# Performance work log

Measured on AMD Instinct MI355X. Metric: run time of the kernel, lower is better.

Reference implementation:

```python
import jax, jax.numpy as jnp
import numpy as np

N_NODES = 65536
N_EDGES = 524288
N_GRAPHS = 512
G_NODES = 10000
NUM_DISEASES = 2000
IN_DIM = 128
HID = 256  # 2 * IN_DIM (z_emb concat feat)
D_FEAT = 512
C_FEAT = 512
MAX_Z = 4000


def setup_inputs() -> dict:
    key = jax.random.key(0)
    ks = jax.random.split(key, 20)
    rn = lambda k, shape: jax.random.normal(k, shape, dtype=jnp.float32) * 0.05
    return {
        "z": jax.random.randint(ks[0], (N_NODES,), 0, MAX_Z),
        "node_id": jnp.sort(jax.random.randint(ks[1], (N_NODES,), 0, G_NODES)),
        "src": jax.random.randint(ks[2], (N_EDGES,), 0, N_NODES),
        "dst": jax.random.randint(ks[3], (N_EDGES,), 0, N_NODES),
        "graph_ids": jnp.sort(jax.random.randint(ks[4], (N_NODES,), 0, N_GRAPHS)),
        "z_table": rn(ks[5], (MAX_Z, IN_DIM)),
        "d_feat_tab": rn(ks[6], (G_NODES, D_FEAT)),
        "c_feat_tab": rn(ks[7], (G_NODES, C_FEAT)),
        "Wd": rn(ks[8], (D_FEAT, IN_DIM)),
        "Wc": rn(ks[9], (C_FEAT, IN_DIM)),
        "gin_W1": rn(ks[10], (HID, HID)), "gin_b1": jnp.zeros((HID,), jnp.float32),
        "gin_W2": rn(ks[11], (HID, HID)), "gin_b2": jnp.zeros((HID,), jnp.float32),
        "sage_Wself": rn(ks[12], (HID, HID)),
        "sage_Wneigh": rn(ks[13], (HID, HID)),
        "sage_b": jnp.zeros((HID,), jnp.float32),
        "lin1_W": rn(ks[14], (HID, HID)), "lin1_b": jnp.zeros((HID,), jnp.float32),
        "lin2_W": rn(ks[15], (HID, 1)), "lin2_b": jnp.zeros((1,), jnp.float32),
    }


def reference(z, node_id, src, dst, graph_ids, z_table, d_feat_tab, c_feat_tab,
              Wd, Wc, gin_W1, gin_b1, gin_W2, gin_b2,
              sage_Wself, sage_Wneigh, sage_b, lin1_W, lin1_b, lin2_W, lin2_b):
    # --- input feature construction (Model.forward) ---
    z_emb = z_table[z]                               # [N, IN_DIM]
    d_proj = d_feat_tab[node_id] @ Wd                # d_fc (bias=False)
    c_proj = c_feat_tab[node_id] @ Wc                # c_fc (bias=False)
    disease = (node_id <= NUM_DISEASES)[:, None]
    # node_id is sorted -> masked concat order == node order
    feat = jnp.where(disease, d_proj, c_proj)        # [N, IN_DIM]
    x = jnp.concatenate([z_emb, feat], axis=1)       # [N, HID]
    # --- GINConv: sum aggregation, eps=0, mlp = Lin->ReLU->Lin ---
    agg = jax.ops.segment_sum(x[src], dst, num_segments=N_NODES)
    h = x + agg
    h = jax.nn.relu(h @ gin_W1 + gin_b1) @ gin_W2 + gin_b2
    # --- SAGEConv('mean'): fc_self(h) + fc_neigh(mean_neighbors) + bias ---
    deg = jax.ops.segment_sum(jnp.ones((N_EDGES,), h.dtype), dst, num_segments=N_NODES)
    mean_n = jax.ops.segment_sum(h[src], dst, num_segments=N_NODES) / jnp.maximum(deg, 1.0)[:, None]
    h = h @ sage_Wself + mean_n @ sage_Wneigh + sage_b
    # --- per-graph max pooling readout ---
    g = jax.ops.segment_max(h, graph_ids, num_segments=N_GRAPHS, indices_are_sorted=True)
    g = jnp.where(jnp.isfinite(g), g, 0.0)           # guard empty graphs
    # --- head: Linear -> ReLU -> (dropout p=0, eval) -> Linear ---
    h = jax.nn.relu(g @ lin1_W + lin1_b)
    return h @ lin2_W + lin2_b                       # [N_GRAPHS, 1]
```

## Files before the change

kernel.cpp:

```cpp
#include <hip/hip_runtime.h>
#include <hip/hip_bf16.h>

#define N_NODES     65536
#define N_EDGES     524288
#define N_GRAPHS    512
#define G_NODES_N   10000
#define NUM_DIS     2000
#define IN_DIM      128
#define HID         256
#define D_FEAT      512
#define MAX_Z       4000

typedef _Float16 half8 __attribute__((ext_vector_type(8)));
typedef float    f32x4 __attribute__((ext_vector_type(4)));

typedef __attribute__((address_space(1))) const void as1_void;
typedef __attribute__((address_space(3))) void       as3_void;

__global__ __launch_bounds__(256) void prep_kernel(
    const float* __restrict__ Ws, const float* __restrict__ Wn,
    const float* __restrict__ Wd, const float* __restrict__ Wc,
    const float* __restrict__ W1, const float* __restrict__ W2,
    const float* __restrict__ z_table,
    const int* __restrict__ z, const int* __restrict__ node_id,
    _Float16* __restrict__ WsT, _Float16* __restrict__ WnT,
    _Float16* __restrict__ WdT, _Float16* __restrict__ WcT,
    _Float16* __restrict__ W12P, _Float16* __restrict__ zt16,
    int2* __restrict__ zn2, int* __restrict__ cnt, int* __restrict__ flags)
{
    const int b = blockIdx.x;
    const int tid = threadIdx.x;
    if (b < 64) {
        __shared__ float tile[64][65];
        const float* W; _Float16* T; int K, N, k0, n0;
        if (b < 32) {
            const int mat = b >> 4, t = b & 15;
            K = HID; N = HID; k0 = (t >> 2) * 64; n0 = (t & 3) * 64;
            W = (mat == 0) ? Ws : Wn;
            T = (mat == 0) ? WsT : WnT;
        } else {
            const int bb = b - 32;
            const int mat = bb >> 4, t = bb & 15;
            K = D_FEAT; N = IN_DIM; k0 = (t >> 1) * 64; n0 = (t & 1) * 64;
            W = (mat == 0) ? Wd : Wc;
            T = (mat == 0) ? WdT : WcT;
        }
        const int tx = tid & 63, ty = tid >> 6;
        #pragma unroll
        for (int r = 0; r < 64; r += 4)
            tile[r + ty][tx] = W[(size_t)(k0 + r + ty) * N + n0 + tx];
        __syncthreads();
        #pragma unroll
        for (int c = 0; c < 64; c += 4)
            T[(size_t)(n0 + c + ty) * K + k0 + tx] = (_Float16)tile[tx][c + ty];
    } else if (b < 576) {
        const int bb = b - 64;
        const int mat = bb >> 8;
        const int k = bb & 255;
        const int n = tid;
        const float* W = mat ? W2 : W1;
        const float v = W[(size_t)k * HID + n];
        const size_t idx = (size_t)(mat * 8 + (k >> 5)) * 8192
                         + (size_t)((((k >> 3) & 3) * 256 + n) * 8 + (k & 7));
        W12P[idx] = (_Float16)v;
    } else if (b < 826) {
        const size_t base = ((size_t)(b - 576) * 256 + tid) * 8;
        const float4 f0 = *(const float4*)(z_table + base);
        const float4 f1 = *(const float4*)(z_table + base + 4);
        half8 h;
        h[0]=(_Float16)f0.x; h[1]=(_Float16)f0.y; h[2]=(_Float16)f0.z; h[3]=(_Float16)f0.w;
        h[4]=(_Float16)f1.x; h[5]=(_Float16)f1.y; h[6]=(_Float16)f1.z; h[7]=(_Float16)f1.w;
        *(half8*)(zt16 + base) = h;
    } else if (b < 890) {
        const int base = (b - 826) * 1024 + tid * 4;
        *(int4*)(cnt + base) = make_int4(0, 0, 0, 0);
        if (b == 826 && tid < 128) flags[tid] = 0;
    } else {
        const int i = (b - 890) * 256 + tid;
        zn2[i] = make_int2(z[i] << 8, node_id[i] << 8);
    }
}

__global__ __launch_bounds__(256) void proj_hist_kernel(
    const float* __restrict__ dtab, const float* __restrict__ ctab,
    const _Float16* __restrict__ WdT, const _Float16* __restrict__ WcT,
    _Float16* __restrict__ proj,
    const int* __restrict__ dst, int* __restrict__ cnt)
{
    const int blk = blockIdx.x;
    if (blk >= 79) {
        const int e = (blk - 79) * 256 + threadIdx.x;
        if (e < N_EDGES) atomicAdd(&cnt[dst[e]], 1);
        return;
    }
    __shared__ _Float16 Alds[128 * 40];
    __shared__ _Float16 Blds[128 * 40];
    const float* tab; const _Float16* WT; int base, M, bm;
    if (blk < 16) { tab = dtab; WT = WdT; base = 0;           M = NUM_DIS + 1;             bm = blk * 128; }
    else          { tab = ctab; WT = WcT; base = NUM_DIS + 1; M = G_NODES_N - NUM_DIS - 1; bm = (blk - 16) * 128; }
    const int tid  = threadIdx.x;
    const int wave = tid >> 6, lane = tid & 63;
    const int q    = lane >> 4, l16 = lane & 15;
    const int mbase = (wave & 1) * 64, nbase = (wave >> 1) * 64;
    const int r = tid >> 1, s = tid & 1;

    f32x4 acc[4][4] = {};

    for (int kc = 0; kc < 16; ++kc) {
        const int k0 = kc * 32;
        const int arow = min(bm + r, M - 1);
        const float* gA = tab + (size_t)(base + arow) * D_FEAT + k0 + s * 16;
        const _Float16* gB = WT + (size_t)r * D_FEAT + k0 + s * 16;
        const float4 f0 = ((const float4*)gA)[0];
        const float4 f1 = ((const float4*)gA)[1];
        const float4 f2 = ((const float4*)gA)[2];
        const float4 f3 = ((const float4*)gA)[3];
        const half8 hb0 = *(const half8*)gB;
        const half8 hb1 = *(const half8*)(gB + 8);
        half8 h0, h1;
        h0[0]=(_Float16)f0.x; h0[1]=(_Float16)f0.y; h0[2]=(_Float16)f0.z; h0[3]=(_Float16)f0.w;
        h0[4]=(_Float16)f1.x; h0[5]=(_Float16)f1.y; h0[6]=(_Float16)f1.z; h0[7]=(_Float16)f1.w;
        h1[0]=(_Float16)f2.x; h1[1]=(_Float16)f2.y; h1[2]=(_Float16)f2.z; h1[3]=(_Float16)f2.w;
        h1[4]=(_Float16)f3.x; h1[5]=(_Float16)f3.y; h1[6]=(_Float16)f3.z; h1[7]=(_Float16)f3.w;
        __syncthreads();
        *(half8*)&Alds[r * 40 + s * 16]     = h0;
        *(half8*)&Alds[r * 40 + s * 16 + 8] = h1;
        *(half8*)&Blds[r * 40 + s * 16]     = hb0;
        *(half8*)&Blds[r * 40 + s * 16 + 8] = hb1;
        __syncthreads();
        half8 a[4], b[4];
        #pragma unroll
        for (int i = 0; i < 4; ++i)
            a[i] = *(const half8*)&Alds[(mbase + i * 16 + l16) * 40 + q * 8];
        #pragma unroll
        for (int j = 0; j < 4; ++j)
            b[j] = *(const half8*)&Blds[(nbase + j * 16 + l16) * 40 + q * 8];
        #pragma unroll
        for (int i = 0; i < 4; ++i)
            #pragma unroll
            for (int j = 0; j < 4; ++j)
                acc[i][j] = __builtin_amdgcn_mfma_f32_16x16x32_f16(a[i], b[j], acc[i][j], 0, 0, 0);
    }

    #pragma unroll
    for (int j = 0; j < 4; ++j) {
        const int colg = nbase + j * 16 + l16;
        #pragma unroll
        for (int i = 0; i < 4; ++i) {
            #pragma unroll
            for (int rr = 0; rr < 4; ++rr) {
                const int row = bm + mbase + i * 16 + q * 4 + rr;
                if (row < M)
                    proj[(size_t)(base + row) * IN_DIM + colg] = (_Float16)acc[i][j][rr];
            }
        }
    }
}

__global__ __launch_bounds__(256) void scan_fused_kernel(
    const int* __restrict__ cnt, int* __restrict__ row_ptr,
    int* __restrict__ fill, int* __restrict__ flags,
    const int2* __restrict__ zn2, int2* __restrict__ pzn,
    int2* __restrict__ prbe, int* __restrict__ pnode,
    int* __restrict__ bhist)
{
    __shared__ int a[256], b[256];
    __shared__ int sums[64];
    __shared__ int segbase;
    __shared__ int hist[64];
    __shared__ int pos[64];
    const int t = threadIdx.x;
    const int blk = blockIdx.x;
    const int base = blk * 1024 + t * 4;
    const int4 c = *(const int4*)(cnt + base);
    const int s = c.x + c.y + c.z + c.w;
    a[t] = s;
    if (t < 64) hist[t] = 0;
    __syncthreads();
    int* in = a; int* out = b;
    for (int off = 1; off < 256; off <<= 1) {
        out[t] = in[t] + ((t >= off) ? in[t - off] : 0);
        __syncthreads();
        int* tmp = in; in = out; out = tmp;
    }
    if (t == 0) {
        atomicExch(&flags[64 + blk], in[255]);
        __threadfence();
        atomicAdd(&flags[0], 1);
        while (atomicAdd(&flags[0], 0) < 64) {}
    }
    __syncthreads();
    if (t < 64) sums[t] = atomicAdd(&flags[64 + t], 0);
    __syncthreads();
    if (t == 0) {
        int pfx = 0;
        for (int i = 0; i < blk; ++i) pfx += sums[i];
        segbase = pfx;
        if (blk == 63) {
            int tot = pfx;
            for (int i = blk; i < 64; ++i) tot += sums[i];
            row_ptr[N_NODES] = tot;
        }
    }
    __syncthreads();
    const int run = in[t] - s + segbase;
    int4 r;
    r.x = run; r.y = run + c.x; r.z = r.y + c.y; r.w = r.z + c.z;
    *(int4*)(row_ptr + base) = r;
    *(int4*)(fill + base) = r;

    const int bk0 = min(c.x, 63), bk1 = min(c.y, 63);
    const int bk2 = min(c.z, 63), bk3 = min(c.w, 63);
    atomicAdd(&hist[bk0], 1); atomicAdd(&hist[bk1], 1);
    atomicAdd(&hist[bk2], 1); atomicAdd(&hist[bk3], 1);
    __syncthreads();
    if (t < 64) bhist[blk * 64 + t] = hist[t];
    __threadfence();
    if (t == 0) {
        atomicAdd(&flags[1], 1);
        while (atomicAdd(&flags[1], 0) < 64) {}
    }
    __syncthreads();
    if (t < 64) {
        int pre = 0, tot = 0;
        for (int i = 0; i < 64; ++i) {
            const int v = atomicAdd(&bhist[i * 64 + t], 0);
            if (i < blk) pre += v;
            tot += v;
        }
        hist[t] = tot;
        pos[t] = pre;
    }
    __syncthreads();
    if (t == 0) {
        int run2 = 0;
        for (int i = 0; i < 64; ++i) { const int tt = hist[i]; hist[i] = run2; run2 += tt; }
    }
    __syncthreads();
    if (t < 64) pos[t] = hist[t] + pos[t];
    __syncthreads();
    const int begs[4] = { r.x, r.y, r.z, r.w };
    const int ends[4] = { r.y, r.z, r.w, r.w + c.w };
    const int bks[4]  = { bk0, bk1, bk2, bk3 };
    #pragma unroll
    for (int k = 0; k < 4; ++k) {
        const int p = atomicAdd(&pos[bks[k]], 1);
        pzn[p]   = zn2[base + k];
        prbe[p]  = make_int2(begs[k], ends[k]);
        pnode[p] = base + k;
    }
}

__global__ __launch_bounds__(256) void scatter_kernel(
    const int* __restrict__ src, const int* __restrict__ dst,
    const int2* __restrict__ zn2,
    int* __restrict__ fill, int* __restrict__ col, int2* __restrict__ colzn)
{
    const int e = blockIdx.x * 256 + threadIdx.x;
    if (e < N_EDGES) {
        const int s = src[e];
        const int pos = atomicAdd(&fill[dst[e]], 1);
        col[pos] = s;
        colzn[pos] = zn2[s];
    }
}

__global__ __launch_bounds__(256) void gin_fused_kernel(
    const int2* __restrict__ prbe, const int2* __restrict__ colzn,
    const int2* __restrict__ pzn, const int* __restrict__ pnode,
    const _Float16* __restrict__ zt16, const _Float16* __restrict__ proj,
    const _Float16* __restrict__ W12P,
    const float* __restrict__ b1, const float* __restrict__ b2,
    _Float16* __restrict__ H)
{
    __shared__ _Float16 Apanel[64 * 264];
    __shared__ _Float16 Blds[8192];
    __shared__ int prows[64];

    const int bm   = blockIdx.x * 64;
    const int tid  = threadIdx.x;
    const int wave = tid >> 6, lane = tid & 63;
    const int q    = lane >> 4, l16 = lane & 15;
    const int nbase = wave * 64;
    const int sb   = wave * 256 + lane;

    if (tid < 64) prows[tid] = pnode[bm + tid];

    #pragma unroll
    for (int tt = 0; tt < 4; ++tt) {
        const int seg = (wave * 4 + tt) * 64 + lane;
        __builtin_amdgcn_global_load_lds((as1_void*)(W12P + seg * 8),
            (as3_void*)&Blds[(wave * 4 + tt) * 64 * 8], 16, 0, 0);
    }

    {
        const int p = tid & 7;
        const char* ztb = (const char*)zt16 + p * 32;
        const char* prb = (const char*)proj + p * 32;
        #pragma unroll 1
        for (int pass = 0; pass < 2; ++pass) {
            const int r  = (tid >> 3) + (pass << 5);
            const int gr = bm + r;
            const int2 be = prbe[gr];
            const int beg = be.x, end = be.y;
            float za[16], pa[16];
            {
                const int2 zn = pzn[gr];
                const half8* zp = (const half8*)(ztb + zn.x);
                const half8* pp = (const half8*)(prb + zn.y);
                const half8 z0 = zp[0], z1 = zp[1], p0 = pp[0], p1 = pp[1];
                #pragma unroll
                for (int i = 0; i < 8; ++i) {
                    za[i] = (float)z0[i]; za[8 + i] = (float)z1[i];
                    pa[i] = (float)p0[i]; pa[8 + i] = (float)p1[i];
                }
            }
            int e = beg;
            int2 iA, iB, iC, iD;
            if (e + 4 <= end) {
                iA = colzn[e]; iB = colzn[e + 1]; iC = colzn[e + 2]; iD = colzn[e + 3];
            }
            for (; e + 4 <= end; e += 4) {
                const half8* zpA = (const half8*)(ztb + iA.x);
                const half8* ppA = (const half8*)(prb + iA.y);
                const half8* zpB = (const half8*)(ztb + iB.x);
                const half8* ppB = (const half8*)(prb + iB.y);
                const half8* zpC = (const half8*)(ztb + iC.x);
                const half8* ppC = (const half8*)(prb + iC.y);
                const half8* zpD = (const half8*)(ztb + iD.x);
                const half8* ppD = (const half8*)(prb + iD.y);
                const half8 zA0 = zpA[0], zA1 = zpA[1], pA0 = ppA[0], pA1 = ppA[1];
                const half8 zB0 = zpB[0], zB1 = zpB[1], pB0 = ppB[0], pB1 = ppB[1];
                const half8 zC0 = zpC[0], zC1 = zpC[1], pC0 = ppC[0], pC1 = ppC[1];
                const half8 zD0 = zpD[0], zD1 = zpD[1], pD0 = ppD[0], pD1 = ppD[1];
                if (e + 8 <= end) {
                    iA = colzn[e + 4]; iB = colzn[e + 5];
                    iC = colzn[e + 6]; iD = colzn[e + 7];
                }
                #pragma unroll
                for (int i = 0; i < 8; ++i) {
                    za[i]     += ((float)zA0[i] + (float)zB0[i]) + ((float)zC0[i] + (float)zD0[i]);
                    za[8 + i] += ((float)zA1[i] + (float)zB1[i]) + ((float)zC1[i] + (float)zD1[i]);
                    pa[i]     += ((float)pA0[i] + (float)pB0[i]) + ((float)pC0[i] + (float)pD0[i]);
                    pa[8 + i] += ((float)pA1[i] + (float)pB1[i]) + ((float)pC1[i] + (float)pD1[i]);
                }
            }
            for (; e + 2 <= end; e += 2) {
                const int2 jA = colzn[e];
                const int2 jB = colzn[e + 1];
                const half8* zpA = (const half8*)(ztb + jA.x);
                const half8* ppA = (const half8*)(prb + jA.y);
                const half8* zpB = (const half8*)(ztb + jB.x);
                const half8* ppB = (const half8*)(prb + jB.y);
                const half8 zA0 = zpA[0], zA1 = zpA[1], pA0 = ppA[0], pA1 = ppA[1];
                const half8 zB0 = zpB[0], zB1 = zpB[1], pB0 = ppB[0], pB1 = ppB[1];
                #pragma unroll
                for (int i = 0; i < 8; ++i) {
                    za[i]     += (float)zA0[i] + (float)zB0[i];
                    za[8 + i] += (float)zA1[i] + (float)zB1[i];
                    pa[i]     += (float)pA0[i] + (float)pB0[i];
                    pa[8 + i] += (float)pA1[i] + (float)pB1[i];
                }
            }
            if (e < end) {
                const int2 jA = colzn[e];
                const half8* zp = (const half8*)(ztb + jA.x);
                const half8* pp = (const half8*)(prb + jA.y);
                const half8 z0 = zp[0], z1 = zp[1], p0 = pp[0], p1 = pp[1];
                #pragma unroll
                for (int i = 0; i < 8; ++i) {
                    za[i] += (float)z0[i]; za[8 + i] += (float)z1[i];
                    pa[i] += (float)p0[i]; pa[8 + i] += (float)p1[i];
                }
            }
            half8 oz0, oz1, op0, op1;
            #pragma unroll
            for (int i = 0; i < 8; ++i) {
                oz0[i] = (_Float16)za[i];     oz1[i] = (_Float16)za[8 + i];
                op0[i] = (_Float16)pa[i];     op1[i] = (_Float16)pa[8 + i];
            }
            *(half8*)&Apanel[r * 264 + p * 16]           = oz0;
            *(half8*)&Apanel[r * 264 + p * 16 + 8]       = oz1;
            *(half8*)&Apanel[r * 264 + 128 + p * 16]     = op0;
            *(half8*)&Apanel[r * 264 + 128 + p * 16 + 8] = op1;
        }
    }
    __syncthreads();

    half8 pf0, pf1, pf2, pf3;
    auto pfetch = [&](int c) {
        const _Float16* s = W12P + (size_t)c * 8192 + (size_t)sb * 8;
        pf0 = *(const half8*)(s);
        pf1 = *(const half8*)(s + 512);
        pf2 = *(const half8*)(s + 1024);
        pf3 = *(const half8*)(s + 1536);
    };
    pfetch(1);

    f32x4 acc[4][4] = {};
    for (int c = 0; c < 16; ++c) {
        const int kl = (c & 7) * 32;
        half8 a[4], b[4];
        #pragma unroll
        for (int i = 0; i < 4; ++i)
            a[i] = *(const half8*)&Apanel[(i * 16 + l16) * 264 + kl + q * 8];
        #pragma unroll
        for (int j = 0; j < 4; ++j)
            b[j] = *(const half8*)&Blds[(q * 256 + nbase + j * 16 + l16) * 8];
        #pragma unroll
        for (int i = 0; i < 4; ++i)
            #pragma unroll
            for (int j = 0; j < 4; ++j)
                acc[i][j] = __builtin_amdgcn_mfma_f32_16x16x32_f16(a[i], b[j], acc[i][j], 0, 0, 0);
        if (c == 15) break;
        __syncthreads();
        *(half8*)&Blds[sb * 8]         = pf0;
        *(half8*)&Blds[(sb + 64) * 8]  = pf1;
        *(half8*)&Blds[(sb + 128) * 8] = pf2;
        *(half8*)&Blds[(sb + 192) * 8] = pf3;
        if (c == 7) {
            #pragma unroll
            for (int j = 0; j < 4; ++j) {
                const int colg = nbase + j * 16 + l16;
                const float bv = b1[colg];
                #pragma unroll
                for (int i = 0; i < 4; ++i)
                    #pragma unroll
                    for (int rr = 0; rr < 4; ++rr) {
                        const float v = fmaxf(acc[i][j][rr] + bv, 0.0f);
                        Apanel[(i * 16 + q * 4 + rr) * 264 + colg] = (_Float16)v;
                        acc[i][j][rr] = 0.0f;
                    }
            }
        }
        if (c < 14) pfetch(c + 2);
        __syncthreads();
    }

    #pragma unroll
    for (int j = 0; j < 4; ++j) {
        const int colg = nbase + j * 16 + l16;
        const float bv = b2[colg];
        #pragma unroll
        for (int i = 0; i < 4; ++i)
            #pragma unroll
            for (int rr = 0; rr < 4; ++rr) {
                const int rowl = i * 16 + q * 4 + rr;
                H[(size_t)prows[rowl] * HID + colg] = (_Float16)(acc[i][j][rr] + bv);
            }
    }
}

__global__ __launch_bounds__(256) void csr_agg_kernel(
    const int2* __restrict__ prbe, const int* __restrict__ pnode,
    const int* __restrict__ col,
    const _Float16* __restrict__ F, _Float16* __restrict__ OUT)
{
    const int t = blockIdx.x * 256 + threadIdx.x;
    const int i = t >> 5;
    const int q = t & 31;
    const int2 be = prbe[i];
    const int beg = be.x, end = be.y;
    float acc[8] = {0.f,0.f,0.f,0.f,0.f,0.f,0.f,0.f};
    int e = beg;
    for (; e + 8 <= end; e += 8) {
        const int s0 = col[e],     s1 = col[e + 1];
        const int s2 = col[e + 2], s3 = col[e + 3];
        const int s4 = col[e + 4], s5 = col[e + 5];
        const int s6 = col[e + 6], s7 = col[e + 7];
        const half8 v0 = *(const half8*)(F + (size_t)s0 * HID + q * 8);
        const half8 v1 = *(const half8*)(F + (size_t)s1 * HID + q * 8);
        const half8 v2 = *(const half8*)(F + (size_t)s2 * HID + q * 8);
        const half8 v3 = *(const half8*)(F + (size_t)s3 * HID + q * 8);
        const half8 v4 = *(const half8*)(F + (size_t)s4 * HID + q * 8);
        const half8 v5 = *(const half8*)(F + (size_t)s5 * HID + q * 8);
        const half8 v6 = *(const half8*)(F + (size_t)s6 * HID + q * 8);
        const half8 v7 = *(const half8*)(F + (size_t)s7 * HID + q * 8);
        #pragma unroll
        for (int k = 0; k < 8; ++k)
            acc[k] += (((float)v0[k] + (float)v1[k]) + ((float)v2[k] + (float)v3[k]))
                    + (((float)v4[k] + (float)v5[k]) + ((float)v6[k] + (float)v7[k]));
    }
    for (; e + 4 <= end; e += 4) {
        const int s0 = col[e],     s1 = col[e + 1];
        const int s2 = col[e + 2], s3 = col[e + 3];
        const half8 v0 = *(const half8*)(F + (size_t)s0 * HID + q * 8);
        const half8 v1 = *(const half8*)(F + (size_t)s1 * HID + q * 8);
        const half8 v2 = *(const half8*)(F + (size_t)s2 * HID + q * 8);
        const half8 v3 = *(const half8*)(F + (size_t)s3 * HID + q * 8);
        #pragma unroll
        for (int k = 0; k < 8; ++k)
            acc[k] += ((float)v0[k] + (float)v1[k]) + ((float)v2[k] + (float)v3[k]);
    }
    for (; e < end; ++e) {
        const half8 v0 = *(const half8*)(F + (size_t)col[e] * HID + q * 8);
        #pragma unroll
        for (int k = 0; k < 8; ++k) acc[k] += (float)v0[k];
    }
    const float rs = 1.0f / fmaxf((float)(end - beg), 1.0f);
    half8 o;
    #pragma unroll
    for (int k = 0; k < 8; ++k) o[k] = (_Float16)(acc[k] * rs);
    const int d = pnode[i];
    *(half8*)(OUT + (size_t)d * HID + q * 8) = o;
}

__global__ __launch_bounds__(256) void mfma_gemm_kernel(
    const _Float16* __restrict__ A1, const _Float16* __restrict__ A2,
    const _Float16* __restrict__ B1T, const _Float16* __restrict__ B2T,
    const float* __restrict__ bias, _Float16* __restrict__ Ch)
{
    __shared__ _Float16 Alds[128 * 32];
    __shared__ _Float16 Blds[128 * 32];
    const int bm   = blockIdx.x * 128;
    const int bn   = blockIdx.y * 128;
    const int tid  = threadIdx.x;
    const int wave = tid >> 6, lane = tid & 63;
    const int q    = lane >> 4, l16 = lane & 15;
    const int mbase = (wave & 1) * 64, nbase = (wave >> 1) * 64;

    const int i0 = wave * 128 + lane;
    const int i1 = i0 + 64;
    const int r0 = i0 >> 2, s0 = i0 & 3;
    const int r1 = i1 >> 2, s1 = i1 & 3;

    half8 pa0, pa1, pb0, pb1;
    auto pfetch = [&](int kc) {
        const int k0 = (kc & 7) * 32;
        const _Float16* Ab = (kc < 8) ? A1 : A2;
        const _Float16* Bb = (kc < 8) ? B1T : B2T;
        pa0 = *(const half8*)(Ab + (size_t)(bm + r0) * HID + k0 + s0 * 8);
        pa1 = *(const half8*)(Ab + (size_t)(bm + r1) * HID + k0 + s1 * 8);
        pb0 = *(const half8*)(Bb + (size_t)(bn + r0) * HID + k0 + s0 * 8);
        pb1 = *(const half8*)(Bb + (size_t)(bn + r1) * HID + k0 + s1 * 8);
    };
    pfetch(0);

    f32x4 acc[4][4] = {};

    for (int kc = 0; kc < 16; ++kc) {
        __syncthreads();
        *(half8*)&Alds[i0 * 8] = pa0;
        *(half8*)&Alds[i1 * 8] = pa1;
        *(half8*)&Blds[i0 * 8] = pb0;
        *(half8*)&Blds[i1 * 8] = pb1;
        if (kc < 15) pfetch(kc + 1);
        __syncthreads();
        half8 a[4], b[4];
        #pragma unroll
        for (int i = 0; i < 4; ++i)
            a[i] = *(const half8*)&Alds[(mbase + i * 16 + l16) * 32 + q * 8];
        #pragma unroll
        for (int j = 0; j < 4; ++j)
            b[j] = *(const half8*)&Blds[(nbase + j * 16 + l16) * 32 + q * 8];
        #pragma unroll
        for (int i = 0; i < 4; ++i)
            #pragma unroll
            for (int j = 0; j < 4; ++j)
                acc[i][j] = __builtin_amdgcn_mfma_f32_16x16x32_f16(a[i], b[j], acc[i][j], 0, 0, 0);
    }

    #pragma unroll
    for (int j = 0; j < 4; ++j) {
        const int colg = bn + nbase + j * 16 + l16;
        const float bv = bias[colg];
        #pragma unroll
        for (int i = 0; i < 4; ++i) {
            #pragma unroll
            for (int rr = 0; rr < 4; ++rr) {
                const int rowg = bm + mbase + i * 16 + q * 4 + rr;
                Ch[(size_t)rowg * HID + colg] = (_Float16)(acc[i][j][rr] + bv);
            }
        }
    }
}

__global__ __launch_bounds__(256) void pool_head_kernel(
    const _Float16* __restrict__ H2, const int* __restrict__ gid,
    const float* __restrict__ W1, const float* __restrict__ b1,
    const float* __restrict__ W2, const float* __restrict__ b2,
    float* __restrict__ out)
{
    const int g = blockIdx.x;
    const int tid = threadIdx.x;
    int lo = 0, hi = N_NODES;
    while (lo < hi) { const int mid = (lo + hi) >> 1; if (gid[mid] < g) lo = mid + 1; else hi = mid; }
    const int start = lo;
    hi = N_NODES;
    while (lo < hi) { const int mid = (lo + hi) >> 1; if (gid[mid] < g + 1) lo = mid + 1; else hi = mid; }
    const int end = lo;

    const int rowofs = tid >> 5;
    const int q = tid & 31;
    float m8[8];
    #pragma unroll
    for (int k = 0; k < 8; ++k) m8[k] = -INFINITY;
    for (int i = start + rowofs; i < end; i += 8) {
        const half8 v = *(const half8*)(H2 + (size_t)i * HID + q * 8);
        #pragma unroll
        for (int k = 0; k < 8; ++k) m8[k] = fmaxf(m8[k], (float)v[k]);
    }
    __shared__ float part[8][256];
    #pragma unroll
    for (int k = 0; k < 8; ++k) part[rowofs][q * 8 + k] = m8[k];
    __syncthreads();
    __shared__ float row[HID];
    __shared__ float red[HID];
    const int j = tid;
    float m = part[0][j];
    #pragma unroll
    for (int r = 1; r < 8; ++r) m = fmaxf(m, part[r][j]);
    row[j] = (m == -INFINITY) ? 0.0f : m;
    __syncthreads();
    float acc = b1[j];
    #pragma unroll 8
    for (int k = 0; k < HID; ++k)
        acc = fmaf(row[k], W1[k * HID + j], acc);
    acc = fmaxf(acc, 0.f);
    red[j] = acc * W2[j];
    __syncthreads();
    for (int s = 128; s > 0; s >>= 1) {
        if (j < s) red[j] += red[j + s];
        __syncthreads();
    }
    if (j == 0) out[g] = red[0] + b2[0];
}

extern "C" void kernel_launch(void* const* d_in, const int* in_sizes, int n_in,
                              void* d_out, int out_size, void* d_ws, size_t ws_size,
                              hipStream_t stream)
{
    const int*   z         = (const int*)d_in[0];
    const int*   node_id   = (const int*)d_in[1];
    const int*   src       = (const int*)d_in[2];
    const int*   dst       = (const int*)d_in[3];
    const int*   graph_ids = (const int*)d_in[4];
    const float* z_table   = (const float*)d_in[5];
    const float* d_feat    = (const float*)d_in[6];
    const float* c_feat    = (const float*)d_in[7];
    const float* Wd        = (const float*)d_in[8];
    const float* Wc        = (const float*)d_in[9];
    const float* gin_W1    = (const float*)d_in[10];
    const float* gin_b1    = (const float*)d_in[11];
    const float* gin_W2    = (const float*)d_in[12];
    const float* gin_b2    = (const float*)d_in[13];
    const float* sage_Wself  = (const float*)d_in[14];
    const float* sage_Wneigh = (const float*)d_in[15];
    const float* sage_b    = (const float*)d_in[16];
    const float* lin1_W    = (const float*)d_in[17];
    const float* lin1_b    = (const float*)d_in[18];
    const float* lin2_W    = (const float*)d_in[19];
    const float* lin2_b    = (const float*)d_in[20];
    float* out = (float*)d_out;

    const size_t NH = (size_t)N_NODES * HID;
    char* wsb = (char*)d_ws;
    _Float16* Hh   = (_Float16*)wsb;                     wsb += NH * 2;
    _Float16* AGGh = (_Float16*)wsb;                     wsb += NH * 2;
    _Float16* H2h  = (_Float16*)wsb;                     wsb += NH * 2;
    _Float16* projh= (_Float16*)wsb;                     wsb += (size_t)G_NODES_N * IN_DIM * 2;
    _Float16* W12P = (_Float16*)wsb;                     wsb += 16 * 8192 * 2;
    _Float16* WsT  = (_Float16*)wsb;                     wsb += HID * HID * 2;
    _Float16* WnT  = (_Float16*)wsb;                     wsb += HID * HID * 2;
    _Float16* WdT  = (_Float16*)wsb;                     wsb += D_FEAT * IN_DIM * 2;
    _Float16* WcT  = (_Float16*)wsb;                     wsb += D_FEAT * IN_DIM * 2;
    _Float16* zt16 = (_Float16*)wsb;                     wsb += (size_t)MAX_Z * IN_DIM * 2;
    int2* zn2      = (int2*)wsb;                         wsb += (size_t)N_NODES * 8;
    int2* colzn    = (int2*)wsb;                         wsb += (size_t)(N_EDGES + 8) * 8;
    int2* pzn      = (int2*)wsb;                         wsb += (size_t)N_NODES * 8;
    int2* prbe     = (int2*)wsb;                         wsb += (size_t)N_NODES * 8;
    int* pnode     = (int*)wsb;                          wsb += (size_t)N_NODES * 4;
    int* bhist     = (int*)wsb;                          wsb += 64 * 64 * 4;
    int* row_ptr   = (int*)wsb;                          wsb += (N_NODES + 4) * 4;
    int* cnt       = (int*)wsb;                          wsb += N_NODES * 4;
    int* fill      = (int*)wsb;                          wsb += N_NODES * 4;
    int* col       = (int*)wsb;                          wsb += N_EDGES * 4;
    int* flags     = (int*)wsb;                          wsb += 128 * 4;

    prep_kernel<<<1146, 256, 0, stream>>>(
        sage_Wself, sage_Wneigh, Wd, Wc, gin_W1, gin_W2, z_table, z, node_id,
        WsT, WnT, WdT, WcT, W12P, zt16, zn2, cnt, flags);

    proj_hist_kernel<<<79 + N_EDGES / 256, 256, 0, stream>>>(
        d_feat, c_feat, WdT, WcT, projh, dst, cnt);

    scan_fused_kernel<<<64, 256, 0, stream>>>(
        cnt, row_ptr, fill, flags, zn2, pzn, prbe, pnode, bhist);
    scatter_kernel<<<N_EDGES / 256, 256, 0, stream>>>(src, dst, zn2, fill, col, colzn);

    gin_fused_kernel<<<N_NODES / 64, 256, 0, stream>>>(
        prbe, colzn, pzn, pnode, zt16, projh, W12P, gin_b1, gin_b2, Hh);

    csr_agg_kernel<<<(N_NODES * 32) / 256, 256, 0, stream>>>(
        prbe, pnode, col, Hh, AGGh);

    dim3 ggrid(N_NODES / 128, HID / 128);
    mfma_gemm_kernel<<<ggrid, 256, 0, stream>>>(Hh, AGGh, WsT, WnT, sage_b, H2h);

    pool_head_kernel<<<N_GRAPHS, 256, 0, stream>>>(
        H2h, graph_ids, lin1_W, lin1_b, lin2_W, lin2_b, out);
}
```

Baseline: 348.6 us.

## Split GIN gather out of fused MLP kernel into separate gather pass

Moves the neighbor-sum aggregation of the GIN layer out of the fused gather+MLP kernel into a dedicated gather kernel that uses 16 lanes per node, with z-embedding and projection halves handled by different lanes. The aggregated fp16 rows are written to a new workspace buffer and then loaded into LDS by the MLP kernel. The aim is more parallelism and better latency hiding for the irregular gathers, which previously ran with only 8 threads per row inside the LDS-heavy MLP kernel. The cost is an extra global round trip of a 65536x256 fp16 buffer and one more kernel launch.

```diff
diff --git a/kernel.cpp b/kernel.cpp
--- a/kernel.cpp
+++ b/kernel.cpp
@@ -265,10 +265,68 @@
     }
 }
 
-__global__ __launch_bounds__(256) void gin_fused_kernel(
-    const int2* __restrict__ prbe, const int2* __restrict__ colzn,
-    const int2* __restrict__ pzn, const int* __restrict__ pnode,
+__global__ __launch_bounds__(256, 6) void gather_kernel(
+    const int2* __restrict__ prbe, const int2* __restrict__ pzn,
+    const int2* __restrict__ colzn,
     const _Float16* __restrict__ zt16, const _Float16* __restrict__ proj,
+    _Float16* __restrict__ AGG)
+{
+    const int i = blockIdx.x * 16 + (threadIdx.x >> 4);
+    const int l = threadIdx.x & 15;
+    const bool isz = (l < 8);
+    const char* tab = isz ? (const char*)zt16 : (const char*)proj;
+    const int loff = (l & 7) * 32;
+    const int2 be = prbe[i];
+    const int2 zn = pzn[i];
+    float acc[16];
+    {
+        const half8* sp = (const half8*)(tab + (isz ? zn.x : zn.y) + loff);
+        const half8 v0 = sp[0], v1 = sp[1];
+        #pragma unroll
+        for (int k = 0; k < 8; ++k) { acc[k] = (float)v0[k]; acc[8 + k] = (float)v1[k]; }
+    }
+    int e = be.x;
+    const int end = be.y;
+    int2 iA, iB, iC, iD;
+    if (e + 4 <= end) {
+        iA = colzn[e]; iB = colzn[e + 1]; iC = colzn[e + 2]; iD = colzn[e + 3];
+    }
+    for (; e + 4 <= end; e += 4) {
+        const half8* sA = (const half8*)(tab + (isz ? iA.x : iA.y) + loff);
+        const half8* sB = (const half8*)(tab + (isz ? iB.x : iB.y) + loff);
+        const half8* sC = (const half8*)(tab + (isz ? iC.x : iC.y) + loff);
+        const half8* sD = (const half8*)(tab + (isz ? iD.x : iD.y) + loff);
+        const half8 a0 = sA[0], a1 = sA[1];
+        const half8 b0 = sB[0], b1 = sB[1];
+        const half8 c0 = sC[0], c1 = sC[1];
+        const half8 d0 = sD[0], d1 = sD[1];
+        if (e + 8 <= end) {
+            iA = colzn[e + 4]; iB = colzn[e + 5];
+            iC = colzn[e + 6]; iD = colzn[e + 7];
+        }
+        #pragma unroll
+        for (int k = 0; k < 8; ++k) {
+            acc[k]     += ((float)a0[k] + (float)b0[k]) + ((float)c0[k] + (float)d0[k]);
+            acc[8 + k] += ((float)a1[k] + (float)b1[k]) + ((float)c1[k] + (float)d1[k]);
+        }
+    }
+    for (; e < end; ++e) {
+        const int2 j = colzn[e];
+        const half8* s = (const half8*)(tab + (isz ? j.x : j.y) + loff);
+        const half8 v0 = s[0], v1 = s[1];
+        #pragma unroll
+        for (int k = 0; k < 8; ++k) { acc[k] += (float)v0[k]; acc[8 + k] += (float)v1[k]; }
+    }
+    half8 o0, o1;
+    #pragma unroll
+    for (int k = 0; k < 8; ++k) { o0[k] = (_Float16)acc[k]; o1[k] = (_Float16)acc[8 + k]; }
+    _Float16* dst = AGG + (size_t)i * 256 + l * 16;
+    *(half8*)dst = o0;
+    *(half8*)(dst + 8) = o1;
+}
+
+__global__ __launch_bounds__(256) void gin_mlp_kernel(
+    const _Float16* __restrict__ AGG, const int* __restrict__ pnode,
     const _Float16* __restrict__ W12P,
     const float* __restrict__ b1, const float* __restrict__ b2,
     _Float16* __restrict__ H)
@@ -294,96 +352,14 @@
     }
 
     {
-        const int p = tid & 7;
-        const char* ztb = (const char*)zt16 + p * 32;
-        const char* prb = (const char*)proj + p * 32;
-        #pragma unroll 1
-        for (int pass = 0; pass < 2; ++pass) {
-            const int r  = (tid >> 3) + (pass << 5);
-            const int gr = bm + r;
-            const int2 be = prbe[gr];
-            const int beg = be.x, end = be.y;
-            float za[16], pa[16];
-            {
-                const int2 zn = pzn[gr];
-                const half8* zp = (const half8*)(ztb + zn.x);
-                const half8* pp = (const half8*)(prb + zn.y);
-                const half8 z0 = zp[0], z1 = zp[1], p0 = pp[0], p1 = pp[1];
-                #pragma unroll
-                for (int i = 0; i < 8; ++i) {
-                    za[i] = (float)z0[i]; za[8 + i] = (float)z1[i];
-                    pa[i] = (float)p0[i]; pa[8 + i] = (float)p1[i];
-                }
-            }
-            int e = beg;
-            int2 iA, iB, iC, iD;
-            if (e + 4 <= end) {
-                iA = colzn[e]; iB = colzn[e + 1]; iC = colzn[e + 2]; iD = colzn[e + 3];
-            }
-            for (; e + 4 <= end; e += 4) {
-                const half8* zpA = (const half8*)(ztb + iA.x);
-                const half8* ppA = (const half8*)(prb + iA.y);
-                const half8* zpB = (const half8*)(ztb + iB.x);
-                const half8* ppB = (const half8*)(prb + iB.y);
-                const half8* zpC = (const half8*)(ztb + iC.x);
-                const half8* ppC = (const half8*)(prb + iC.y);
-                const half8* zpD = (const half8*)(ztb + iD.x);
-                const half8* ppD = (const half8*)(prb + iD.y);
-                const half8 zA0 = zpA[0], zA1 = zpA[1], pA0 = ppA[0], pA1 = ppA[1];
-                const half8 zB0 = zpB[0], zB1 = zpB[1], pB0 = ppB[0], pB1 = ppB[1];
-                const half8 zC0 = zpC[0], zC1 = zpC[1], pC0 = ppC[0], pC1 = ppC[1];
-                const half8 zD0 = zpD[0], zD1 = zpD[1], pD0 = ppD[0], pD1 = ppD[1];
-                if (e + 8 <= end) {
-                    iA = colzn[e + 4]; iB = colzn[e + 5];
-                    iC = colzn[e + 6]; iD = colzn[e + 7];
-                }
-                #pragma unroll
-                for (int i = 0; i < 8; ++i) {
-                    za[i]     += ((float)zA0[i] + (float)zB0[i]) + ((float)zC0[i] + (float)zD0[i]);
-                    za[8 + i] += ((float)zA1[i] + (float)zB1[i]) + ((float)zC1[i] + (float)zD1[i]);
-                    pa[i]     += ((float)pA0[i] + (float)pB0[i]) + ((float)pC0[i] + (float)pD0[i]);
-                    pa[8 + i] += ((float)pA1[i] + (float)pB1[i]) + ((float)pC1[i] + (float)pD1[i]);
-                }
-            }
-            for (; e + 2 <= end; e += 2) {
-                const int2 jA = colzn[e];
-                const int2 jB = colzn[e + 1];
-                const half8* zpA = (const half8*)(ztb + jA.x);
-                const half8* ppA = (const half8*)(prb + jA.y);
-                const half8* zpB = (const half8*)(ztb + jB.x);
-                const half8* ppB = (const half8*)(prb + jB.y);
-                const half8 zA0 = zpA[0], zA1 = zpA[1], pA0 = ppA[0], pA1 = ppA[1];
-                const half8 zB0 = zpB[0], zB1 = zpB[1], pB0 = ppB[0], pB1 = ppB[1];
-                #pragma unroll
-                for (int i = 0; i < 8; ++i) {
-                    za[i]     += (float)zA0[i] + (float)zB0[i];
-                    za[8 + i] += (float)zA1[i] + (float)zB1[i];
-                    pa[i]     += (float)pA0[i] + (float)pB0[i];
-                    pa[8 + i] += (float)pA1[i] + (float)pB1[i];
-                }
-            }
-            if (e < end) {
-                const int2 jA = colzn[e];
-                const half8* zp = (const half8*)(ztb + jA.x);
-                const half8* pp = (const half8*)(prb + jA.y);
-                const half8 z0 = zp[0], z1 = zp[1], p0 = pp[0], p1 = pp[1];
-                #pragma unroll
-                for (int i = 0; i < 8; ++i) {
-                    za[i] += (float)z0[i]; za[8 + i] += (float)z1[i];
-                    pa[i] += (float)p0[i]; pa[8 + i] += (float)p1[i];
-                }
-            }
-            half8 oz0, oz1, op0, op1;
-            #pragma unroll
-            for (int i = 0; i < 8; ++i) {
-                oz0[i] = (_Float16)za[i];     oz1[i] = (_Float16)za[8 + i];
-                op0[i] = (_Float16)pa[i];     op1[i] = (_Float16)pa[8 + i];
-            }
-            *(half8*)&Apanel[r * 264 + p * 16]           = oz0;
-            *(half8*)&Apanel[r * 264 + p * 16 + 8]       = oz1;
-            *(half8*)&Apanel[r * 264 + 128 + p * 16]     = op0;
-            *(half8*)&Apanel[r * 264 + 128 + p * 16 + 8] = op1;
-        }
+        const int ar = tid >> 2, acs = (tid & 3) * 64;
+        const _Float16* asrc = AGG + (size_t)(bm + ar) * 256 + acs;
+        half8 av[8];
+        #pragma unroll
+        for (int k = 0; k < 8; ++k) av[k] = *(const half8*)(asrc + k * 8);
+        #pragma unroll
+        for (int k = 0; k < 8; ++k)
+            *(half8*)&Apanel[ar * 264 + acs + k * 8] = av[k];
     }
     __syncthreads();
 
@@ -658,6 +634,7 @@
     _Float16* Hh   = (_Float16*)wsb;                     wsb += NH * 2;
     _Float16* AGGh = (_Float16*)wsb;                     wsb += NH * 2;
     _Float16* H2h  = (_Float16*)wsb;                     wsb += NH * 2;
+    _Float16* AGGx = (_Float16*)wsb;                     wsb += NH * 2;
     _Float16* projh= (_Float16*)wsb;                     wsb += (size_t)G_NODES_N * IN_DIM * 2;
     _Float16* W12P = (_Float16*)wsb;                     wsb += 16 * 8192 * 2;
     _Float16* WsT  = (_Float16*)wsb;                     wsb += HID * HID * 2;
@@ -688,8 +665,10 @@
         cnt, row_ptr, fill, flags, zn2, pzn, prbe, pnode, bhist);
     scatter_kernel<<<N_EDGES / 256, 256, 0, stream>>>(src, dst, zn2, fill, col, colzn);
 
-    gin_fused_kernel<<<N_NODES / 64, 256, 0, stream>>>(
-        prbe, colzn, pzn, pnode, zt16, projh, W12P, gin_b1, gin_b2, Hh);
+    gather_kernel<<<N_NODES / 16, 256, 0, stream>>>(
+        prbe, pzn, colzn, zt16, projh, AGGx);
+    gin_mlp_kernel<<<N_NODES / 64, 256, 0, stream>>>(
+        AGGx, pnode, W12P, gin_b1, gin_b2, Hh);
 
     csr_agg_kernel<<<(N_NODES * 32) / 256, 256, 0, stream>>>(
         prbe, pnode, col, Hh, AGGh);
```

New measurement: 351.4 us. No clear change (+0.8%).
